# Performance work log

Hardware: AMD Instinct MI355X
Metric: run time of the kernel (lower is better)

## Reference

```python
import jax, jax.numpy as jnp
import numpy as np

MODEL_DIM = 1024
FF_DIMS = (1024, 2048, 4096)  # max_ff_dim // 2**(num_levels-1-level), floored at model_dim
NUM_LEVELS = 3


def _gelu(x):
    return jax.nn.gelu(x, approximate=False)  # torch nn.GELU default is exact erf GELU


def setup_inputs() -> dict:
    key = jax.random.key(0)
    ks = jax.random.split(key, 20)
    d = MODEL_DIM
    inp = {
        "token_embeddings": jax.random.normal(ks[0], (4, 4096, d), dtype=jnp.float32),
        # importance classifier: Linear(d, d//2) -> GELU -> Linear(d//2, num_levels) -> Softmax
        "Wc1": jax.random.normal(ks[1], (d, d // 2), dtype=jnp.float32) * 0.02,
        "bc1": jnp.zeros((d // 2,), dtype=jnp.float32),
        "Wc2": jax.random.normal(ks[2], (d // 2, NUM_LEVELS), dtype=jnp.float32) * 0.02,
        "bc2": jnp.zeros((NUM_LEVELS,), dtype=jnp.float32),
    }
    # per-level FFN: Linear(d, ff) -> GELU -> Linear(ff, d)
    for lvl, ff in enumerate(FF_DIMS):
        inp[f"W1_{lvl}"] = jax.random.normal(ks[3 + 4 * lvl], (d, ff), dtype=jnp.float32) * 0.02
        inp[f"b1_{lvl}"] = jnp.zeros((ff,), dtype=jnp.float32)
        inp[f"W2_{lvl}"] = jax.random.normal(ks[4 + 4 * lvl], (ff, d), dtype=jnp.float32) * 0.02
        inp[f"b2_{lvl}"] = jnp.zeros((d,), dtype=jnp.float32)
    return inp


def reference(token_embeddings, Wc1, bc1, Wc2, bc2,
              W1_0, b1_0, W2_0, b2_0,
              W1_1, b1_1, W2_1, b2_1,
              W1_2, b1_2, W2_2, b2_2):
    x = token_embeddings  # [B, S, D]
    # importance classifier -> per-token routing level (argmax over softmax probs)
    logits = _gelu(x @ Wc1 + bc1) @ Wc2 + bc2  # [B, S, L]
    probs = jax.nn.softmax(logits, axis=-1)
    levels = jnp.argmax(probs, axis=-1)  # [B, S] int
    # per-level FFN; select per-token output (dense compute + masked select is the
    # jit-friendly equivalent of the gather->MLP->scatter in the original)
    params = ((W1_0, b1_0, W2_0, b2_0), (W1_1, b1_1, W2_1, b2_1), (W1_2, b1_2, W2_2, b2_2))
    out = jnp.zeros_like(x)
    for lvl, (W1, b1, W2, b2) in enumerate(params):
        y = _gelu(x @ W1 + b1) @ W2 + b2  # [B, S, D]
        out = jnp.where((levels == lvl)[..., None], y, out)
    return out
```

## Files before the change

kernel.cpp:

```cpp
#include <hip/hip_runtime.h>
#include <math.h>

#define T_TOTAL 16384
#define DMODEL  1024
#define MARGIN  2.5e-3f

typedef __attribute__((ext_vector_type(8))) _Float16 f16x8;
typedef __attribute__((ext_vector_type(4))) float    f32x4;

#define SEL3(l, a, b, c) ((l) == 0 ? (a) : (l) == 1 ? (b) : (c))

#define CTR_STRIDE 32

__device__ __forceinline__ float gelu_exact(float x) {
    return 0.5f * x * (1.0f + erff(x * 0.7071067811865476f));
}
__device__ __forceinline__ unsigned short f2h(float f) {
    union { _Float16 h; unsigned short s; } c; c.h = (_Float16)f; return c.s;
}
__device__ __forceinline__ float h2f(unsigned short u) {
    union { unsigned short s; _Float16 h; } c; c.s = u; return (float)c.h;
}
__device__ __forceinline__ void gll16(const void* g, void* l) {
    __builtin_amdgcn_global_load_lds(
        (const __attribute__((address_space(1))) unsigned int*)g,
        (__attribute__((address_space(3))) unsigned int*)l, 16, 0, 0);
}

__device__ __forceinline__ int swz_bid() {
    const int b = blockIdx.x;
    const int G = gridDim.x;
    if (G & 63) return b;
    const int x = b & 7, j = b >> 3;
    return (x + 8 * (j >> 3)) * 8 + (j & 7);
}


struct PackP {
    const float* src[7];
    unsigned short* dst[7];
    int K[7], N[7];
    int boff[8];
    const float* X;
    unsigned short* Xh;
    int cvtBlocks;
};

__global__ __launch_bounds__(256) void k_pack_all(PackP p)
{
    if (blockIdx.x < p.cvtBlocks) {
        const size_t i = ((size_t)blockIdx.x * 256 + threadIdx.x) * 8;
        float4 f0 = *(const float4*)(p.X + i);
        float4 f1 = *(const float4*)(p.X + i + 4);
        unsigned short o[8] __attribute__((aligned(16)));
        o[0]=f2h(f0.x); o[1]=f2h(f0.y); o[2]=f2h(f0.z); o[3]=f2h(f0.w);
        o[4]=f2h(f1.x); o[5]=f2h(f1.y); o[6]=f2h(f1.z); o[7]=f2h(f1.w);
        *(uint4*)(p.Xh + i) = *(uint4*)o;
        return;
    }
    const int gb = blockIdx.x - p.cvtBlocks;
    int t = 0;
    while (t < 6 && gb >= p.boff[t + 1]) ++t;
    const int lb = gb - p.boff[t];
    const float* src = p.src[t];
    unsigned short* dst = p.dst[t];
    const int K = p.K[t], N = p.N[t];

    const int ktiles = K >> 5;
    const int nt = lb / ktiles;
    const int kt = lb % ktiles;
    __shared__ float ls[32][129];
    const int tid = threadIdx.x;
    {
        const int c  = tid >> 3;
        const int n0 = (tid & 7) * 16;
        const float* s = src + (size_t)(kt * 32 + c) * N + (size_t)nt * 128 + n0;
#pragma unroll
        for (int v = 0; v < 4; ++v) {
            float4 f = *(const float4*)(s + v * 4);
            ls[c][n0 + v*4 + 0] = f.x; ls[c][n0 + v*4 + 1] = f.y;
            ls[c][n0 + v*4 + 2] = f.z; ls[c][n0 + v*4 + 3] = f.w;
        }
    }
    __syncthreads();
    {
        const int r  = tid >> 1;
        const int c0 = (tid & 1) * 16;
        unsigned short tmp[16] __attribute__((aligned(16)));
#pragma unroll
        for (int c = 0; c < 16; ++c) tmp[c] = f2h(ls[c0 + c][r]);
        unsigned short* d = dst + (size_t)lb * (128 * 32) + r * 32 + c0;
        *(uint4*)(d)     = *(uint4*)&tmp[0];
        *(uint4*)(d + 8) = *(uint4*)&tmp[8];
    }
}

#define KLOOP_BODY(KC, A0, A1, BSR, ASTEP)                                     \
    gll16(A0,        As + w * 1024);                                           \
    gll16(A1,        As + w * 1024 + 512);                                     \
    gll16(BSR,       Bs + w * 1024);                                           \
    gll16(BSR + 512, Bs + w * 1024 + 512);                                     \
    const int sr = (tq >> 1) & 3;                                              \
    int cur = 0;                                                               \
    for (int kt = 0; kt < (KC); ++kt) {                                        \
        const int nxt = cur ^ 1;                                               \
        if (kt + 1 < (KC)) {                                                   \
            gll16(A0 + (size_t)(kt+1) * (ASTEP),       As + nxt * 4096 + w * 1024);        \
            gll16(A1 + (size_t)(kt+1) * (ASTEP),       As + nxt * 4096 + w * 1024 + 512);  \
            gll16(BSR + (size_t)(kt+1) * 4096,         Bs + nxt * 4096 + w * 1024);        \
            gll16(BSR + (size_t)(kt+1) * 4096 + 512,   Bs + nxt * 4096 + w * 1024 + 512);  \
            asm volatile("s_waitcnt vmcnt(4)" ::: "memory");                   \
        } else {                                                               \
            asm volatile("s_waitcnt vmcnt(0)" ::: "memory");                   \
        }                                                                      \
        __builtin_amdgcn_s_barrier();                                          \
        const unsigned short* rA = As + cur * 4096;                            \
        const unsigned short* rB = Bs + cur * 4096;                            \
        f16x8 a[4], b[4];                                                      \
        _Pragma("unroll")                                                      \
        for (int i = 0; i < 4; ++i) a[i] = *(const f16x8*)(rA + (wr*64 + i*16 + tq) * 32 + (q ^ sr) * 8); \
        _Pragma("unroll")                                                      \
        for (int j = 0; j < 4; ++j) b[j] = *(const f16x8*)(rB + (wc*64 + j*16 + tq) * 32 + (q ^ sr) * 8); \
        asm volatile("s_waitcnt lgkmcnt(0)" ::: "memory");                     \
        __builtin_amdgcn_sched_barrier(0);                                     \
        _Pragma("unroll")                                                      \
        for (int i = 0; i < 4; ++i)                                            \
            _Pragma("unroll")                                                  \
            for (int j = 0; j < 4; ++j)                                        \
                acc[i][j] = __builtin_amdgcn_mfma_f32_16x16x32_f16(b[j], a[i], acc[i][j], 0, 0, 0); \
        __builtin_amdgcn_s_barrier();                                          \
        cur = nxt;                                                             \
    }

__global__ __launch_bounds__(256) void k_h(
    const unsigned short* __restrict__ Xh, const unsigned short* __restrict__ Wq,
    const float* __restrict__ bc1, unsigned short* __restrict__ H)
{
    const int bid = swz_bid();
    const int mt = bid >> 2;
    const int nt = bid & 3;
    __shared__ __align__(16) unsigned short As[2 * 128 * 32];
    __shared__ __align__(16) unsigned short Bs[2 * 128 * 32];

    const int tid = threadIdx.x;
    const int w = tid >> 6, ln = tid & 63;
    const int wr = w >> 1, wc = w & 1;
    const int q = ln >> 4, tq = ln & 15;

    f32x4 acc[4][4];
#pragma unroll
    for (int i = 0; i < 4; ++i)
#pragma unroll
        for (int j = 0; j < 4; ++j) acc[i][j] = (f32x4){0.f, 0.f, 0.f, 0.f};

    const int colA  = (((ln & 3) ^ ((ln >> 3) & 3))) * 8;
    const int laneB = (ln >> 2) * 32 + colA;
    const int r0 = mt * 128 + w * 32 + (ln >> 2);
    const unsigned short* a0 = Xh + (size_t)r0 * DMODEL + colA;
    const unsigned short* a1 = a0 + (size_t)16 * DMODEL;
    const unsigned short* bsr = Wq + (size_t)nt * 32 * 4096 + w * 1024 + laneB;

    KLOOP_BODY(32, a0, a1, bsr, 32)

#pragma unroll
    for (int i = 0; i < 4; ++i) {
        const int t = mt * 128 + wr * 64 + i * 16 + tq;
        unsigned short* hrow = H + (size_t)t * 512;
#pragma unroll
        for (int j = 0; j < 4; ++j) {
            const int cb = nt * 128 + wc * 64 + j * 16 + q * 4;
            float4 bv = *(const float4*)(bc1 + cb);
            f32x4 v = acc[i][j];
            unsigned short o[4] __attribute__((aligned(8)));
            o[0] = f2h(gelu_exact(v[0] + bv.x));
            o[1] = f2h(gelu_exact(v[1] + bv.y));
            o[2] = f2h(gelu_exact(v[2] + bv.z));
            o[3] = f2h(gelu_exact(v[3] + bv.w));
            *(uint2*)(hrow + cb) = *(uint2*)o;
        }
    }
}

__global__ __launch_bounds__(256) void k_levels(
    const unsigned short* __restrict__ H, const float* __restrict__ Wc2,
    const float* __restrict__ bc2, int* __restrict__ ctrs,
    int* __restrict__ idxb, int* __restrict__ flaglist)
{
    __shared__ int lvlbuf[64];
    const int tid  = threadIdx.x;
    const int wv   = tid >> 6, lane = tid & 63;
    const int t0   = blockIdx.x * 64;
    const int j0   = lane * 8;

    float wa[8], wb[8], wc[8];
#pragma unroll
    for (int jj = 0; jj < 8; ++jj) {
        const float* wr = Wc2 + (j0 + jj) * 3;
        wa[jj] = wr[0]; wb[jj] = wr[1]; wc[jj] = wr[2];
    }
    const float bz0 = bc2[0], bz1 = bc2[1], bz2 = bc2[2];

    for (int it = 0; it < 16; ++it) {
        const int t = t0 + wv * 16 + it;
        const unsigned short* hrow = H + (size_t)t * 512 + j0;
        unsigned short hu[8] __attribute__((aligned(16)));
        *(uint4*)hu = *(const uint4*)hrow;

        float a0 = 0.f, a1 = 0.f, a2 = 0.f;
#pragma unroll
        for (int jj = 0; jj < 8; ++jj) {
            const float h = h2f(hu[jj]);
            a0 += h * wa[jj]; a1 += h * wb[jj]; a2 += h * wc[jj];
        }
#pragma unroll
        for (int off = 32; off; off >>= 1) {
            a0 += __shfl_xor(a0, off);
            a1 += __shfl_xor(a1, off);
            a2 += __shfl_xor(a2, off);
        }
        if (lane == 0) {
            a0 += bz0; a1 += bz1; a2 += bz2;
            int lvl = 0; float best = a0;
            if (a1 > best) { best = a1; lvl = 1; }
            if (a2 > best) { best = a2; lvl = 2; }
            float second = (lvl == 0) ? fmaxf(a1, a2) : (lvl == 1) ? fmaxf(a0, a2) : fmaxf(a0, a1);
            lvlbuf[wv * 16 + it] = (best - second < MARGIN) ? 3 : lvl;
        }
    }
    __syncthreads();
    if (tid < 64) {
        const int mylvl = lvlbuf[tid];
        const int mytok = t0 + tid;
#pragma unroll
        for (int lvl = 0; lvl < 4; ++lvl) {
            const unsigned long long m = __ballot(mylvl == lvl);
            int base = 0;
            if (tid == 0) {
                const int cnt = __popcll(m);
                if (cnt) base = atomicAdd(&ctrs[lvl * CTR_STRIDE], cnt);
            }
            base = __shfl(base, 0);
            if (mylvl == lvl) {
                const int pos = base + __popcll(m & ((1ull << tid) - 1ull));
                if (lvl < 3) idxb[lvl * T_TOTAL + pos] = mytok;
                else         flaglist[pos] = mytok;
            }
        }
    }
}

__global__ __launch_bounds__(256) void k_exact(
    const float* __restrict__ X, const float* __restrict__ Wc1,
    const float* __restrict__ bc1, const float* __restrict__ Wc2,
    const float* __restrict__ bc2, const int* __restrict__ flaglist,
    const int* __restrict__ flagcnt, int* __restrict__ ctrs,
    int* __restrict__ idxb)
{
    __shared__ float xs[1024][8];
    __shared__ float red[4][8][3];
    const int tid = threadIdx.x;
    const int nflag = flagcnt[0];

    for (int g = blockIdx.x; g * 8 < nflag; g += gridDim.x) {
        {
            const int s   = tid >> 5;
            const int l32 = tid & 31;
            int fi = g * 8 + s; if (fi >= nflag) fi = nflag - 1;
            const float* xr = X + (size_t)flaglist[fi] * DMODEL;
#pragma unroll
            for (int kk = 0; kk < 32; ++kk) {
                const int k = kk * 32 + l32;
                xs[k][s] = xr[k];
            }
        }
        __syncthreads();
        const int j = tid;
        float acc0[8], acc1[8];
#pragma unroll
        for (int s = 0; s < 8; ++s) { acc0[s] = 0.f; acc1[s] = 0.f; }
        for (int k = 0; k < 1024; ++k) {
            float4 xa = *(const float4*)&xs[k][0];
            float4 xb = *(const float4*)&xs[k][4];
            const float w0 = Wc1[(size_t)k * 512 + j];
            const float w1 = Wc1[(size_t)k * 512 + j + 256];
            acc0[0] += xa.x * w0; acc0[1] += xa.y * w0; acc0[2] += xa.z * w0; acc0[3] += xa.w * w0;
            acc0[4] += xb.x * w0; acc0[5] += xb.y * w0; acc0[6] += xb.z * w0; acc0[7] += xb.w * w0;
            acc1[0] += xa.x * w1; acc1[1] += xa.y * w1; acc1[2] += xa.z * w1; acc1[3] += xa.w * w1;
            acc1[4] += xb.x * w1; acc1[5] += xb.y * w1; acc1[6] += xb.z * w1; acc1[7] += xb.w * w1;
        }
        float p[8][3];
        {
            const float b0 = bc1[j], b1 = bc1[j + 256];
            const float* w2a = Wc2 + j * 3;
            const float* w2b = Wc2 + (j + 256) * 3;
#pragma unroll
            for (int s = 0; s < 8; ++s) {
                const float h0v = gelu_exact(acc0[s] + b0);
                const float h1v = gelu_exact(acc1[s] + b1);
                p[s][0] = h0v * w2a[0] + h1v * w2b[0];
                p[s][1] = h0v * w2a[1] + h1v * w2b[1];
                p[s][2] = h0v * w2a[2] + h1v * w2b[2];
            }
        }
#pragma unroll
        for (int off = 32; off; off >>= 1)
#pragma unroll
            for (int s = 0; s < 8; ++s) {
                p[s][0] += __shfl_xor(p[s][0], off);
                p[s][1] += __shfl_xor(p[s][1], off);
                p[s][2] += __shfl_xor(p[s][2], off);
            }
        if ((tid & 63) == 0) {
            const int w = tid >> 6;
#pragma unroll
            for (int s = 0; s < 8; ++s) {
                red[w][s][0] = p[s][0]; red[w][s][1] = p[s][1]; red[w][s][2] = p[s][2];
            }
        }
        __syncthreads();
        if (tid < 8) {
            const int fi = g * 8 + tid;
            if (fi < nflag) {
                float l0 = bc2[0], l1 = bc2[1], l2 = bc2[2];
#pragma unroll
                for (int w = 0; w < 4; ++w) {
                    l0 += red[w][tid][0]; l1 += red[w][tid][1]; l2 += red[w][tid][2];
                }
                int lvl = 0; float best = l0;
                if (l1 > best) { best = l1; lvl = 1; }
                if (l2 > best) { best = l2; lvl = 2; }
                const int tok = flaglist[fi];
                const int pos = atomicAdd(&ctrs[lvl * CTR_STRIDE], 1);
                idxb[lvl * T_TOTAL + pos] = tok;
            }
        }
        __syncthreads();
    }
}

__global__ void k_offsets(const int* __restrict__ ctrs, int* __restrict__ off,
                          int h0, int h1, int h2)
{
    if (threadIdx.x == 0 && blockIdx.x == 0) {
        off[0] = 0;
        off[1] = ctrs[0] * h0;
        off[2] = ctrs[0] * h0 + ctrs[CTR_STRIDE] * h1;
    }
}

struct FfnP1 {
    const unsigned short *Wq0, *Wq1, *Wq2;
    const float *bb0, *bb1, *bb2;
    const int* counts; const int* off; const int* idx;
    int s0, s01;
    int NT0, NT1, NT2;
    int st0, st1, st2;
    int no0;
};

__global__ __launch_bounds__(256) void k_ffn1(
    const unsigned short* __restrict__ Xh, unsigned short* __restrict__ Hmid, FfnP1 p)
{
    const int bid = swz_bid();
    int l, r;
    if (bid < p.s0)       { l = 0; r = bid; }
    else if (bid < p.s01) { l = 1; r = bid - p.s0; }
    else                  { l = 2; r = bid - p.s01; }
    const int NT = SEL3(l, p.NT0, p.NT1, p.NT2);
    const int mt = r / NT, nt = r % NT;
    const int n  = p.counts[l * CTR_STRIDE];
    if (mt * 128 >= n) return;

    const int* idx = p.idx + l * T_TOTAL;
    const unsigned short* Wq = SEL3(l, p.Wq0, p.Wq1, p.Wq2);
    const float* bb = SEL3(l, p.bb0, p.bb1, p.bb2);
    const int stride = SEL3(l, p.st0, p.st1, p.st2);
    const size_t hoff = (size_t)p.off[l];

    __shared__ __align__(16) unsigned short As[2 * 128 * 32];
    __shared__ __align__(16) unsigned short Bs[2 * 128 * 32];

    const int tid = threadIdx.x;
    const int w = tid >> 6, ln = tid & 63;
    const int wr = w >> 1, wc = w & 1;
    const int q = ln >> 4, tq = ln & 15;

    f32x4 acc[4][4];
#pragma unroll
    for (int i = 0; i < 4; ++i)
#pragma unroll
        for (int j = 0; j < 4; ++j) acc[i][j] = (f32x4){0.f, 0.f, 0.f, 0.f};

    int r0 = mt * 128 + w * 32 + (ln >> 2);
    int r1 = r0 + 16;
    if (r0 >= n) r0 = n - 1;
    if (r1 >= n) r1 = n - 1;
    const int colA  = (((ln & 3) ^ ((ln >> 3) & 3))) * 8;
    const int laneB = (ln >> 2) * 32 + colA;
    const unsigned short* a0 = Xh + (size_t)idx[r0] * DMODEL + colA;
    const unsigned short* a1 = Xh + (size_t)idx[r1] * DMODEL + colA;
    const unsigned short* bsr = Wq + (size_t)(p.no0 + nt) * 32 * 4096 + w * 1024 + laneB;

    KLOOP_BODY(32, a0, a1, bsr, 32)

#pragma unroll
    for (int i = 0; i < 4; ++i) {
        const int pp = mt * 128 + wr * 64 + i * 16 + tq;
        if (pp < n) {
            unsigned short* hrow = Hmid + hoff + (size_t)pp * stride;
#pragma unroll
            for (int j = 0; j < 4; ++j) {
                const int cb = nt * 128 + wc * 64 + j * 16 + q * 4;
                float4 bv = *(const float4*)(bb + p.no0 * 128 + cb);
                f32x4 v = acc[i][j];
                unsigned short o[4] __attribute__((aligned(8)));
                o[0] = f2h(gelu_exact(v[0] + bv.x));
                o[1] = f2h(gelu_exact(v[1] + bv.y));
                o[2] = f2h(gelu_exact(v[2] + bv.z));
                o[3] = f2h(gelu_exact(v[3] + bv.w));
                *(uint2*)(hrow + cb) = *(uint2*)o;
            }
        }
    }
}

struct FfnP2 {
    const unsigned short *Wq0, *Wq1, *Wq2;
    const float *bb0, *bb1, *bb2;
    const int* counts; const int* off; const int* idx;
    int s2, s21;
    int st0, st1, st2;
    int kb;
    int kc0, kc1, kc2;
    int nf0, nf1, nf2;
    int accum;
};

__global__ __launch_bounds__(256) void k_ffn2(
    const unsigned short* __restrict__ Hmid, float* __restrict__ out, FfnP2 p)
{
    const int bid = swz_bid();
    int l, r;
    if (bid < p.s2)       { l = 2; r = bid; }
    else if (bid < p.s21) { l = 1; r = bid - p.s2; }
    else                  { l = 0; r = bid - p.s21; }
    const int mt = r >> 3, nt = r & 7;
    const int n  = p.counts[l * CTR_STRIDE];
    if (mt * 128 >= n) return;

    const int* idx = p.idx + l * T_TOTAL;
    const unsigned short* Wq = SEL3(l, p.Wq0, p.Wq1, p.Wq2);
    const float* bb = SEL3(l, p.bb0, p.bb1, p.bb2);
    const int stride = SEL3(l, p.st0, p.st1, p.st2);
    const int KC = SEL3(l, p.kc0, p.kc1, p.kc2);
    const int nf = SEL3(l, p.nf0, p.nf1, p.nf2);
    const size_t hoff = (size_t)p.off[l];

    __shared__ __align__(16) unsigned short As[2 * 128 * 32];
    __shared__ __align__(16) unsigned short Bs[2 * 128 * 32];

    const int tid = threadIdx.x;
    const int w = tid >> 6, ln = tid & 63;
    const int wr = w >> 1, wc = w & 1;
    const int q = ln >> 4, tq = ln & 15;

    f32x4 acc[4][4];
#pragma unroll
    for (int i = 0; i < 4; ++i)
#pragma unroll
        for (int j = 0; j < 4; ++j) acc[i][j] = (f32x4){0.f, 0.f, 0.f, 0.f};

    int r0 = mt * 128 + w * 32 + (ln >> 2);
    int r1 = r0 + 16;
    if (r0 >= n) r0 = n - 1;
    if (r1 >= n) r1 = n - 1;
    const int colA  = (((ln & 3) ^ ((ln >> 3) & 3))) * 8;
    const int laneB = (ln >> 2) * 32 + colA;
    const unsigned short* a0 = Hmid + hoff + (size_t)r0 * stride + colA;
    const unsigned short* a1 = Hmid + hoff + (size_t)r1 * stride + colA;
    const unsigned short* bsr = Wq + ((size_t)nt * nf + p.kb) * 4096 + w * 1024 + laneB;

    KLOOP_BODY(KC, a0, a1, bsr, 32)

#pragma unroll
    for (int i = 0; i < 4; ++i) {
        const int pp = mt * 128 + wr * 64 + i * 16 + tq;
        if (pp < n) {
            float* orow = out + (size_t)idx[pp] * DMODEL;
#pragma unroll
            for (int j = 0; j < 4; ++j) {
                const int cb = nt * 128 + wc * 64 + j * 16 + q * 4;
                f32x4 v = acc[i][j];
                float4 res;
                if (p.accum) {
                    float4 cur4 = *(const float4*)(orow + cb);
                    res.x = cur4.x + v[0]; res.y = cur4.y + v[1];
                    res.z = cur4.z + v[2]; res.w = cur4.w + v[3];
                } else {
                    float4 bv = *(const float4*)(bb + cb);
                    res.x = v[0] + bv.x; res.y = v[1] + bv.y;
                    res.z = v[2] + bv.z; res.w = v[3] + bv.w;
                }
                *(float4*)(orow + cb) = res;
            }
        }
    }
}

extern "C" void kernel_launch(void* const* d_in, const int* in_sizes, int n_in,
                              void* d_out, int out_size, void* d_ws, size_t ws_size,
                              hipStream_t stream)
{
    (void)in_sizes; (void)n_in; (void)out_size;

    const float* X   = (const float*)d_in[0];
    const float* Wc1 = (const float*)d_in[1];
    const float* bc1 = (const float*)d_in[2];
    const float* Wc2 = (const float*)d_in[3];
    const float* bc2 = (const float*)d_in[4];
    const float* W1[3] = {(const float*)d_in[5],  (const float*)d_in[9],  (const float*)d_in[13]};
    const float* b1[3] = {(const float*)d_in[6],  (const float*)d_in[10], (const float*)d_in[14]};
    const float* W2[3] = {(const float*)d_in[7],  (const float*)d_in[11], (const float*)d_in[15]};
    const float* b2[3] = {(const float*)d_in[8],  (const float*)d_in[12], (const float*)d_in[16]};
    float* out = (float*)d_out;
    const int FF[3] = {1024, 2048, 4096};

    char* w = (char*)d_ws;
    size_t o = 0;
    auto take = [&](size_t bytes) -> char* {
        char* p = w + o;
        o = (o + bytes + 255) & ~(size_t)255;
        return p;
    };
    unsigned short* W1p[3]; for (int l = 0; l < 3; ++l) W1p[l] = (unsigned short*)take((size_t)1024 * FF[l] * 2);
    unsigned short* W2p[3]; for (int l = 0; l < 3; ++l) W2p[l] = (unsigned short*)take((size_t)1024 * FF[l] * 2);
    unsigned short* Wc1p = (unsigned short*)take((size_t)1024 * 512 * 2);
    unsigned short* Xh   = (unsigned short*)take((size_t)T_TOTAL * DMODEL * 2);
    unsigned short* H    = (unsigned short*)take((size_t)T_TOTAL * 512 * 2);
    int* flaglist = (int*)take((size_t)T_TOTAL * 4);
    int* idxb     = (int*)take((size_t)3 * T_TOTAL * 4);
    int* ctrs     = (int*)take(1024);
    unsigned short* Hmid = (unsigned short*)(w + o);
    const size_t avail = ws_size > o ? ws_size - o : 0;

    int CHUNK = 256;
    const int cand[4] = {4096, 2048, 1024, 512};
    for (int ci = 0; ci < 4; ++ci)
        if ((size_t)T_TOTAL * cand[ci] * 2 <= avail) { CHUNK = cand[ci]; break; }
    int HC[3]; for (int l = 0; l < 3; ++l) HC[l] = FF[l] < CHUNK ? FF[l] : CHUNK;

    hipMemsetAsync(ctrs, 0, 1024, stream);

    {
        PackP pk;
        int ob = 0, slot = 0;
        auto addpk = [&](const float* s, unsigned short* d2, int K, int N) {
            pk.src[slot] = s; pk.dst[slot] = d2; pk.K[slot] = K; pk.N[slot] = N;
            pk.boff[slot] = ob; ob += (N / 128) * (K / 32); ++slot;
        };
        for (int l = 0; l < 3; ++l) addpk(W1[l], W1p[l], 1024, FF[l]);
        for (int l = 0; l < 3; ++l) addpk(W2[l], W2p[l], FF[l], 1024);
        addpk(Wc1, Wc1p, 1024, 512);
        pk.boff[7] = ob;
        pk.X = X; pk.Xh = Xh;
        pk.cvtBlocks = (T_TOTAL * DMODEL) / (256 * 8);
        k_pack_all<<<pk.cvtBlocks + ob, 256, 0, stream>>>(pk);
    }

    k_h<<<(T_TOTAL / 128) * 4, 256, 0, stream>>>(Xh, Wc1p, bc1, H);
    k_levels<<<T_TOTAL / 64, 256, 0, stream>>>(H, Wc2, bc2, ctrs, idxb, flaglist);
    k_exact<<<128, 256, 0, stream>>>(X, Wc1, bc1, Wc2, bc2, flaglist, ctrs + 96, ctrs, idxb);
    k_offsets<<<1, 64, 0, stream>>>(ctrs, ctrs + 128, HC[0], HC[1], HC[2]);

    const int nchunks = FF[2] / CHUNK;
    for (int c = 0; c < nchunks; ++c) {
        int NTc[3];
        for (int l = 0; l < 3; ++l) {
            int rem = FF[l] - c * CHUNK;
            NTc[l] = rem > 0 ? (rem < CHUNK ? rem : CHUNK) / 128 : 0;
        }
        const int g1_0 = 128 * NTc[0], g1_1 = 128 * NTc[1], g1_2 = 128 * NTc[2];
        const int G1 = g1_0 + g1_1 + g1_2;
        const int g2_0 = NTc[0] ? 1024 : 0, g2_1 = NTc[1] ? 1024 : 0, g2_2 = NTc[2] ? 1024 : 0;
        const int G2 = g2_0 + g2_1 + g2_2;
        if (G1 == 0) continue;

        FfnP1 p1;
        p1.Wq0 = W1p[0]; p1.Wq1 = W1p[1]; p1.Wq2 = W1p[2];
        p1.bb0 = b1[0];  p1.bb1 = b1[1];  p1.bb2 = b1[2];
        p1.counts = ctrs; p1.off = ctrs + 128; p1.idx = idxb;
        p1.s0 = g1_0; p1.s01 = g1_0 + g1_1;
        p1.NT0 = NTc[0]; p1.NT1 = NTc[1]; p1.NT2 = NTc[2];
        p1.st0 = HC[0]; p1.st1 = HC[1]; p1.st2 = HC[2];
        p1.no0 = c * CHUNK / 128;
        k_ffn1<<<G1, 256, 0, stream>>>(Xh, Hmid, p1);

        FfnP2 p2;
        p2.Wq0 = W2p[0]; p2.Wq1 = W2p[1]; p2.Wq2 = W2p[2];
        p2.bb0 = b2[0];  p2.bb1 = b2[1];  p2.bb2 = b2[2];
        p2.counts = ctrs; p2.off = ctrs + 128; p2.idx = idxb;
        p2.s2 = g2_2; p2.s21 = g2_2 + g2_1;
        p2.st0 = HC[0]; p2.st1 = HC[1]; p2.st2 = HC[2];
        p2.kb = c * CHUNK / 32;
        p2.kc0 = NTc[0] * 4; p2.kc1 = NTc[1] * 4; p2.kc2 = NTc[2] * 4;
        p2.nf0 = FF[0] / 32; p2.nf1 = FF[1] / 32; p2.nf2 = FF[2] / 32;
        p2.accum = (c > 0) ? 1 : 0;
        k_ffn2<<<G2, 256, 0, stream>>>(Hmid, out, p2);
    }
}
```

Baseline: 575.8 us.

## Make grouped FFN kernels persistent with grid-stride tile loop

The grouped FFN up- and down-projection kernels are changed into persistent kernels that are launched with at most 1280 blocks and stride over the tile work list. Tiles that fall past each level's token count are skipped cheaply inside the loop instead of costing a full block launch. The aim is to cut block scheduling overhead and idle empty blocks, since the worst-case grid covers all tokens for every level. The cost is that static striding can load-balance unevenly, and work order across the GPU changes, which may affect cache locality.

```diff
diff --git a/kernel.cpp b/kernel.cpp
--- a/kernel.cpp
+++ b/kernel.cpp
@@ -95,18 +95,17 @@
     }
 }
 
-#define KLOOP_BODY(KC, A0, A1, BSR, ASTEP)                                     \
+#define KLOOP_BODY(KC, A0, A1, BSR)                                            \
     gll16(A0,        As + w * 1024);                                           \
     gll16(A1,        As + w * 1024 + 512);                                     \
     gll16(BSR,       Bs + w * 1024);                                           \
     gll16(BSR + 512, Bs + w * 1024 + 512);                                     \
-    const int sr = (tq >> 1) & 3;                                              \
     int cur = 0;                                                               \
     for (int kt = 0; kt < (KC); ++kt) {                                        \
         const int nxt = cur ^ 1;                                               \
         if (kt + 1 < (KC)) {                                                   \
-            gll16(A0 + (size_t)(kt+1) * (ASTEP),       As + nxt * 4096 + w * 1024);        \
-            gll16(A1 + (size_t)(kt+1) * (ASTEP),       As + nxt * 4096 + w * 1024 + 512);  \
+            gll16(A0 + (size_t)(kt+1) * 32,            As + nxt * 4096 + w * 1024);        \
+            gll16(A1 + (size_t)(kt+1) * 32,            As + nxt * 4096 + w * 1024 + 512);  \
             gll16(BSR + (size_t)(kt+1) * 4096,         Bs + nxt * 4096 + w * 1024);        \
             gll16(BSR + (size_t)(kt+1) * 4096 + 512,   Bs + nxt * 4096 + w * 1024 + 512);  \
             asm volatile("s_waitcnt vmcnt(4)" ::: "memory");                   \
@@ -139,13 +138,14 @@
     const int bid = swz_bid();
     const int mt = bid >> 2;
     const int nt = bid & 3;
-    __shared__ __align__(16) unsigned short As[2 * 128 * 32];
-    __shared__ __align__(16) unsigned short Bs[2 * 128 * 32];
+    __shared__ __align__(16) unsigned short As[2 * 4096];
+    __shared__ __align__(16) unsigned short Bs[2 * 4096];
 
     const int tid = threadIdx.x;
     const int w = tid >> 6, ln = tid & 63;
     const int wr = w >> 1, wc = w & 1;
     const int q = ln >> 4, tq = ln & 15;
+    const int sr = (tq >> 1) & 3;
 
     f32x4 acc[4][4];
 #pragma unroll
@@ -160,7 +160,7 @@
     const unsigned short* a1 = a0 + (size_t)16 * DMODEL;
     const unsigned short* bsr = Wq + (size_t)nt * 32 * 4096 + w * 1024 + laneB;
 
-    KLOOP_BODY(32, a0, a1, bsr, 32)
+    KLOOP_BODY(32, a0, a1, bsr)
 
 #pragma unroll
     for (int i = 0; i < 4; ++i) {
@@ -352,7 +352,7 @@
     const unsigned short *Wq0, *Wq1, *Wq2;
     const float *bb0, *bb1, *bb2;
     const int* counts; const int* off; const int* idx;
-    int s0, s01;
+    int s0, s01, total;
     int NT0, NT1, NT2;
     int st0, st1, st2;
     int no0;
@@ -361,64 +361,69 @@
 __global__ __launch_bounds__(256) void k_ffn1(
     const unsigned short* __restrict__ Xh, unsigned short* __restrict__ Hmid, FfnP1 p)
 {
-    const int bid = swz_bid();
-    int l, r;
-    if (bid < p.s0)       { l = 0; r = bid; }
-    else if (bid < p.s01) { l = 1; r = bid - p.s0; }
-    else                  { l = 2; r = bid - p.s01; }
-    const int NT = SEL3(l, p.NT0, p.NT1, p.NT2);
-    const int mt = r / NT, nt = r % NT;
-    const int n  = p.counts[l * CTR_STRIDE];
-    if (mt * 128 >= n) return;
-
-    const int* idx = p.idx + l * T_TOTAL;
-    const unsigned short* Wq = SEL3(l, p.Wq0, p.Wq1, p.Wq2);
-    const float* bb = SEL3(l, p.bb0, p.bb1, p.bb2);
-    const int stride = SEL3(l, p.st0, p.st1, p.st2);
-    const size_t hoff = (size_t)p.off[l];
-
-    __shared__ __align__(16) unsigned short As[2 * 128 * 32];
-    __shared__ __align__(16) unsigned short Bs[2 * 128 * 32];
+    __shared__ __align__(16) unsigned short As[2 * 4096];
+    __shared__ __align__(16) unsigned short Bs[2 * 4096];
 
     const int tid = threadIdx.x;
     const int w = tid >> 6, ln = tid & 63;
     const int wr = w >> 1, wc = w & 1;
     const int q = ln >> 4, tq = ln & 15;
-
-    f32x4 acc[4][4];
-#pragma unroll
-    for (int i = 0; i < 4; ++i)
-#pragma unroll
-        for (int j = 0; j < 4; ++j) acc[i][j] = (f32x4){0.f, 0.f, 0.f, 0.f};
-
-    int r0 = mt * 128 + w * 32 + (ln >> 2);
-    int r1 = r0 + 16;
-    if (r0 >= n) r0 = n - 1;
-    if (r1 >= n) r1 = n - 1;
+    const int sr = (tq >> 1) & 3;
     const int colA  = (((ln & 3) ^ ((ln >> 3) & 3))) * 8;
     const int laneB = (ln >> 2) * 32 + colA;
-    const unsigned short* a0 = Xh + (size_t)idx[r0] * DMODEL + colA;
-    const unsigned short* a1 = Xh + (size_t)idx[r1] * DMODEL + colA;
-    const unsigned short* bsr = Wq + (size_t)(p.no0 + nt) * 32 * 4096 + w * 1024 + laneB;
-
-    KLOOP_BODY(32, a0, a1, bsr, 32)
-
-#pragma unroll
-    for (int i = 0; i < 4; ++i) {
-        const int pp = mt * 128 + wr * 64 + i * 16 + tq;
-        if (pp < n) {
-            unsigned short* hrow = Hmid + hoff + (size_t)pp * stride;
-#pragma unroll
-            for (int j = 0; j < 4; ++j) {
-                const int cb = nt * 128 + wc * 64 + j * 16 + q * 4;
-                float4 bv = *(const float4*)(bb + p.no0 * 128 + cb);
-                f32x4 v = acc[i][j];
-                unsigned short o[4] __attribute__((aligned(8)));
-                o[0] = f2h(gelu_exact(v[0] + bv.x));
-                o[1] = f2h(gelu_exact(v[1] + bv.y));
-                o[2] = f2h(gelu_exact(v[2] + bv.z));
-                o[3] = f2h(gelu_exact(v[3] + bv.w));
-                *(uint2*)(hrow + cb) = *(uint2*)o;
+    const int sbid = swz_bid();
+
+    for (int base = 0; base < p.total; base += gridDim.x) {
+        const int item = base + sbid;
+        if (item >= p.total) continue;
+        int l, r;
+        if (item < p.s0)       { l = 0; r = item; }
+        else if (item < p.s01) { l = 1; r = item - p.s0; }
+        else                   { l = 2; r = item - p.s01; }
+        const int NT = SEL3(l, p.NT0, p.NT1, p.NT2);
+        const int mt = r / NT, nt = r % NT;
+        const int n  = p.counts[l * CTR_STRIDE];
+        if (mt * 128 >= n) continue;
+
+        const int* idx = p.idx + l * T_TOTAL;
+        const unsigned short* Wq = SEL3(l, p.Wq0, p.Wq1, p.Wq2);
+        const float* bb = SEL3(l, p.bb0, p.bb1, p.bb2);
+        const int stride = SEL3(l, p.st0, p.st1, p.st2);
+        const size_t hoff = (size_t)p.off[l];
+
+        int r0 = mt * 128 + w * 32 + (ln >> 2);
+        int r1 = r0 + 16;
+        if (r0 >= n) r0 = n - 1;
+        if (r1 >= n) r1 = n - 1;
+        const unsigned short* a0 = Xh + (size_t)idx[r0] * DMODEL + colA;
+        const unsigned short* a1 = Xh + (size_t)idx[r1] * DMODEL + colA;
+        const unsigned short* bsr = Wq + (size_t)(p.no0 + nt) * 32 * 4096 + w * 1024 + laneB;
+
+        f32x4 acc[4][4];
+#pragma unroll
+        for (int i = 0; i < 4; ++i)
+#pragma unroll
+            for (int j = 0; j < 4; ++j) acc[i][j] = (f32x4){0.f, 0.f, 0.f, 0.f};
+
+        KLOOP_BODY(32, a0, a1, bsr)
+
+#pragma unroll
+        for (int i = 0; i < 4; ++i) {
+            const int pp = mt * 128 + wr * 64 + i * 16 + tq;
+            if (pp < n) {
+                unsigned short* hrow = Hmid + hoff + (size_t)pp * stride;
+#pragma unroll
+                for (int j = 0; j < 4; ++j) {
+                    const int cb = nt * 128 + wc * 64 + j * 16 + q * 4;
+                    float4 bv = *(const float4*)(bb + p.no0 * 128 + cb);
+                    f32x4 v = acc[i][j];
+                    unsigned short o[4] __attribute__((aligned(8)));
+                    o[0] = f2h(gelu_exact(v[0] + bv.x));
+                    o[1] = f2h(gelu_exact(v[1] + bv.y));
+                    o[2] = f2h(gelu_exact(v[2] + bv.z));
+                    o[3] = f2h(gelu_exact(v[3] + bv.w));
+                    *(uint2*)(hrow + cb) = *(uint2*)o;
+                }
             }
         }
     }
@@ -428,7 +433,7 @@
     const unsigned short *Wq0, *Wq1, *Wq2;
     const float *bb0, *bb1, *bb2;
     const int* counts; const int* off; const int* idx;
-    int s2, s21;
+    int s2, s21, total;
     int st0, st1, st2;
     int kb;
     int kc0, kc1, kc2;
@@ -439,69 +444,74 @@
 __global__ __launch_bounds__(256) void k_ffn2(
     const unsigned short* __restrict__ Hmid, float* __restrict__ out, FfnP2 p)
 {
-    const int bid = swz_bid();
-    int l, r;
-    if (bid < p.s2)       { l = 2; r = bid; }
-    else if (bid < p.s21) { l = 1; r = bid - p.s2; }
-    else                  { l = 0; r = bid - p.s21; }
-    const int mt = r >> 3, nt = r & 7;
-    const int n  = p.counts[l * CTR_STRIDE];
-    if (mt * 128 >= n) return;
-
-    const int* idx = p.idx + l * T_TOTAL;
-    const unsigned short* Wq = SEL3(l, p.Wq0, p.Wq1, p.Wq2);
-    const float* bb = SEL3(l, p.bb0, p.bb1, p.bb2);
-    const int stride = SEL3(l, p.st0, p.st1, p.st2);
-    const int KC = SEL3(l, p.kc0, p.kc1, p.kc2);
-    const int nf = SEL3(l, p.nf0, p.nf1, p.nf2);
-    const size_t hoff = (size_t)p.off[l];
-
-    __shared__ __align__(16) unsigned short As[2 * 128 * 32];
-    __shared__ __align__(16) unsigned short Bs[2 * 128 * 32];
+    __shared__ __align__(16) unsigned short As[2 * 4096];
+    __shared__ __align__(16) unsigned short Bs[2 * 4096];
 
     const int tid = threadIdx.x;
     const int w = tid >> 6, ln = tid & 63;
     const int wr = w >> 1, wc = w & 1;
     const int q = ln >> 4, tq = ln & 15;
-
-    f32x4 acc[4][4];
-#pragma unroll
-    for (int i = 0; i < 4; ++i)
-#pragma unroll
-        for (int j = 0; j < 4; ++j) acc[i][j] = (f32x4){0.f, 0.f, 0.f, 0.f};
-
-    int r0 = mt * 128 + w * 32 + (ln >> 2);
-    int r1 = r0 + 16;
-    if (r0 >= n) r0 = n - 1;
-    if (r1 >= n) r1 = n - 1;
+    const int sr = (tq >> 1) & 3;
     const int colA  = (((ln & 3) ^ ((ln >> 3) & 3))) * 8;
     const int laneB = (ln >> 2) * 32 + colA;
-    const unsigned short* a0 = Hmid + hoff + (size_t)r0 * stride + colA;
-    const unsigned short* a1 = Hmid + hoff + (size_t)r1 * stride + colA;
-    const unsigned short* bsr = Wq + ((size_t)nt * nf + p.kb) * 4096 + w * 1024 + laneB;
-
-    KLOOP_BODY(KC, a0, a1, bsr, 32)
-
-#pragma unroll
-    for (int i = 0; i < 4; ++i) {
-        const int pp = mt * 128 + wr * 64 + i * 16 + tq;
-        if (pp < n) {
-            float* orow = out + (size_t)idx[pp] * DMODEL;
-#pragma unroll
-            for (int j = 0; j < 4; ++j) {
-                const int cb = nt * 128 + wc * 64 + j * 16 + q * 4;
-                f32x4 v = acc[i][j];
-                float4 res;
-                if (p.accum) {
-                    float4 cur4 = *(const float4*)(orow + cb);
-                    res.x = cur4.x + v[0]; res.y = cur4.y + v[1];
-                    res.z = cur4.z + v[2]; res.w = cur4.w + v[3];
-                } else {
-                    float4 bv = *(const float4*)(bb + cb);
-                    res.x = v[0] + bv.x; res.y = v[1] + bv.y;
-                    res.z = v[2] + bv.z; res.w = v[3] + bv.w;
+    const int sbid = swz_bid();
+
+    for (int base = 0; base < p.total; base += gridDim.x) {
+        const int item = base + sbid;
+        if (item >= p.total) continue;
+        int l, r;
+        if (item < p.s2)       { l = 2; r = item; }
+        else if (item < p.s21) { l = 1; r = item - p.s2; }
+        else                   { l = 0; r = item - p.s21; }
+        const int mt = r >> 3, nt = r & 7;
+        const int n  = p.counts[l * CTR_STRIDE];
+        if (mt * 128 >= n) continue;
+
+        const int* idx = p.idx + l * T_TOTAL;
+        const unsigned short* Wq = SEL3(l, p.Wq0, p.Wq1, p.Wq2);
+        const float* bb = SEL3(l, p.bb0, p.bb1, p.bb2);
+        const int stride = SEL3(l, p.st0, p.st1, p.st2);
+        const int KC = SEL3(l, p.kc0, p.kc1, p.kc2);
+        const int nf = SEL3(l, p.nf0, p.nf1, p.nf2);
+        const size_t hoff = (size_t)p.off[l];
+
+        int r0 = mt * 128 + w * 32 + (ln >> 2);
+        int r1 = r0 + 16;
+        if (r0 >= n) r0 = n - 1;
+        if (r1 >= n) r1 = n - 1;
+        const unsigned short* a0 = Hmid + hoff + (size_t)r0 * stride + colA;
+        const unsigned short* a1 = Hmid + hoff + (size_t)r1 * stride + colA;
+        const unsigned short* bsr = Wq + ((size_t)nt * nf + p.kb) * 4096 + w * 1024 + laneB;
+
+        f32x4 acc[4][4];
+#pragma unroll
+        for (int i = 0; i < 4; ++i)
+#pragma unroll
+            for (int j = 0; j < 4; ++j) acc[i][j] = (f32x4){0.f, 0.f, 0.f, 0.f};
+
+        KLOOP_BODY(KC, a0, a1, bsr)
+
+#pragma unroll
+        for (int i = 0; i < 4; ++i) {
+            const int pp = mt * 128 + wr * 64 + i * 16 + tq;
+            if (pp < n) {
+                float* orow = out + (size_t)idx[pp] * DMODEL;
+#pragma unroll
+                for (int j = 0; j < 4; ++j) {
+                    const int cb = nt * 128 + wc * 64 + j * 16 + q * 4;
+                    f32x4 v = acc[i][j];
+                    float4 res;
+                    if (p.accum) {
+                        float4 cur4 = *(const float4*)(orow + cb);
+                        res.x = cur4.x + v[0]; res.y = cur4.y + v[1];
+                        res.z = cur4.z + v[2]; res.w = cur4.w + v[3];
+                    } else {
+                        float4 bv = *(const float4*)(bb + cb);
+                        res.x = v[0] + bv.x; res.y = v[1] + bv.y;
+                        res.z = v[2] + bv.z; res.w = v[3] + bv.w;
+                    }
+                    *(float4*)(orow + cb) = res;
                 }
-                *(float4*)(orow + cb) = res;
             }
         }
     }
@@ -524,6 +534,7 @@
     const float* b2[3] = {(const float*)d_in[8],  (const float*)d_in[12], (const float*)d_in[16]};
     float* out = (float*)d_out;
     const int FF[3] = {1024, 2048, 4096};
+    const int PERSIST = 1280;
 
     char* w = (char*)d_ws;
     size_t o = 0;
@@ -589,22 +600,22 @@
         p1.Wq0 = W1p[0]; p1.Wq1 = W1p[1]; p1.Wq2 = W1p[2];
         p1.bb0 = b1[0];  p1.bb1 = b1[1];  p1.bb2 = b1[2];
         p1.counts = ctrs; p1.off = ctrs + 128; p1.idx = idxb;
-        p1.s0 = g1_0; p1.s01 = g1_0 + g1_1;
+        p1.s0 = g1_0; p1.s01 = g1_0 + g1_1; p1.total = G1;
         p1.NT0 = NTc[0]; p1.NT1 = NTc[1]; p1.NT2 = NTc[2];
         p1.st0 = HC[0]; p1.st1 = HC[1]; p1.st2 = HC[2];
         p1.no0 = c * CHUNK / 128;
-        k_ffn1<<<G1, 256, 0, stream>>>(Xh, Hmid, p1);
+        k_ffn1<<<(G1 < PERSIST ? G1 : PERSIST), 256, 0, stream>>>(Xh, Hmid, p1);
 
         FfnP2 p2;
         p2.Wq0 = W2p[0]; p2.Wq1 = W2p[1]; p2.Wq2 = W2p[2];
         p2.bb0 = b2[0];  p2.bb1 = b2[1];  p2.bb2 = b2[2];
         p2.counts = ctrs; p2.off = ctrs + 128; p2.idx = idxb;
-        p2.s2 = g2_2; p2.s21 = g2_2 + g2_1;
+        p2.s2 = g2_2; p2.s21 = g2_2 + g2_1; p2.total = G2;
         p2.st0 = HC[0]; p2.st1 = HC[1]; p2.st2 = HC[2];
         p2.kb = c * CHUNK / 32;
         p2.kc0 = NTc[0] * 4; p2.kc1 = NTc[1] * 4; p2.kc2 = NTc[2] * 4;
         p2.nf0 = FF[0] / 32; p2.nf1 = FF[1] / 32; p2.nf2 = FF[2] / 32;
         p2.accum = (c > 0) ? 1 : 0;
-        k_ffn2<<<G2, 256, 0, stream>>>(Hmid, out, p2);
-    }
-}
+        k_ffn2<<<(G2 < PERSIST ? G2 : PERSIST), 256, 0, stream>>>(Hmid, out, p2);
+    }
+}
```

Result: slower. 648.8 us (+12.7%).
